# Kernel tuning notes

Hardware: AMD Instinct MI355X
Metric: run time of the kernel (lower is better)

Reference implementation:

```python
import jax, jax.numpy as jnp
import numpy as np

V, E, H, B, T = 32000, 256, 512, 64, 24

def setup_inputs() -> dict:
    key = jax.random.key(0)
    ks = jax.random.split(key, 24)
    def n(k, shape, s=0.02):
        return jax.random.normal(k, shape, dtype=jnp.float32) * s
    inp = {
        "question_feat": n(ks[0], (B, H), 1.0),
        "image_feat": n(ks[1], (B, H), 1.0),
        "answer_seq": jax.random.randint(ks[2], (B, T), 0, V),
        "embedding": n(ks[3], (V, E)),
        "attn_W": n(ks[4], (H, 3 * H)),
        "attn_b": jnp.zeros((H,), jnp.float32),
        "v_W": n(ks[5], (1, H)),
        "fc_W": n(ks[6], (V, H)),
        "fc_b": jnp.zeros((V,), jnp.float32),
    }
    in_sizes = [E + 2 * H, H, H]  # layer0 sees cat(embed, context)=1280
    for l in range(3):
        inp[f"W_ih{l}"] = n(ks[7 + 4 * l], (4 * H, in_sizes[l]))
        inp[f"W_hh{l}"] = n(ks[8 + 4 * l], (4 * H, H))
        inp[f"b_ih{l}"] = jnp.zeros((4 * H,), jnp.float32)
        inp[f"b_hh{l}"] = jnp.zeros((4 * H,), jnp.float32)
    return inp

def _lstm_cell(x, h, c, W_ih, W_hh, b_ih, b_hh):
    # torch gate order: i, f, g, o
    g = x @ W_ih.T + b_ih + h @ W_hh.T + b_hh
    i, f, gg, o = jnp.split(g, 4, axis=-1)
    c_new = jax.nn.sigmoid(f) * c + jax.nn.sigmoid(i) * jnp.tanh(gg)
    h_new = jax.nn.sigmoid(o) * jnp.tanh(c_new)
    return h_new, c_new

def reference(question_feat, image_feat, answer_seq, embedding, attn_W, attn_b, v_W,
              fc_W, fc_b,
              W_ih0, W_hh0, b_ih0, b_hh0,
              W_ih1, W_hh1, b_ih1, b_hh1,
              W_ih2, W_hh2, b_ih2, b_hh2):
    combined = jnp.concatenate([question_feat, image_feat], axis=1)  # [B, 2H]
    x = embedding[answer_seq]            # [B, T, E]
    xs = jnp.swapaxes(x, 0, 1)           # [T, B, E]
    Ws = ((W_ih0, W_hh0, b_ih0, b_hh0),
          (W_ih1, W_hh1, b_ih1, b_hh1),
          (W_ih2, W_hh2, b_ih2, b_hh2))

    def step(carry, x_t):
        h, c, prev_attn = carry          # h, c: [3, B, H]; prev_attn: [B, H]
        energy = jnp.tanh(jnp.concatenate([prev_attn, combined], axis=1) @ attn_W.T + attn_b)
        aw = jax.nn.softmax(energy @ v_W.T, axis=1)  # [B, 1] (softmax over singleton, faithful to source)
        ctx = aw * combined                          # [B, 2H]
        cur = jnp.concatenate([x_t, ctx], axis=1)    # [B, E+2H]
        hs, cs = [], []
        for l in range(3):
            nh, nc = _lstm_cell(cur, h[l], c[l], *Ws[l])
            hs.append(nh); cs.append(nc); cur = nh
        logits = cur @ fc_W.T + fc_b                 # [B, V]
        return (jnp.stack(hs), jnp.stack(cs), cur), logits

    hdim = question_feat.shape[1]
    bsz = question_feat.shape[0]
    h0 = jnp.zeros((3, bsz, hdim), question_feat.dtype)
    c0 = jnp.zeros((3, bsz, hdim), question_feat.dtype)
    _, outs = jax.lax.scan(step, (h0, c0, question_feat), xs)
    return jnp.swapaxes(outs, 0, 1)  # [B, T, V]
```

## Files before the change

### kernel.cpp

```cpp
#include <hip/hip_runtime.h>
#include <hip/hip_bf16.h>
#include <stdint.h>


typedef short bf16x8 __attribute__((ext_vector_type(8)));
typedef float f32x4 __attribute__((ext_vector_type(4)));

#define NLSTM 96
#define NTILE_N 250
#define HSLOT 32768

__device__ __forceinline__ unsigned short f2b(float f) {
    uint32_t u = __builtin_bit_cast(uint32_t, f);
    uint32_t r = u + 0x7FFFu + ((u >> 16) & 1u);
    return (unsigned short)(r >> 16);
}
__device__ __forceinline__ float fsig(float x) {
    float e = __expf(-x);
    return __builtin_amdgcn_rcpf(1.0f + e);
}
__device__ __forceinline__ float ftanh(float x) {
    float e = __expf(-2.0f * x);
    return (1.0f - e) * __builtin_amdgcn_rcpf(1.0f + e);
}

__global__ __launch_bounds__(256) void prep(
    const float* __restrict__ Whh0,
    const float* __restrict__ Wih1, const float* __restrict__ Whh1,
    const float* __restrict__ Wih2, const float* __restrict__ Whh2,
    unsigned short* __restrict__ Wpk,
    const float* __restrict__ qf,
    const float* __restrict__ imf,
    const int* __restrict__ seq,
    const float* __restrict__ emb,
    unsigned short* __restrict__ X,
    unsigned int* __restrict__ flags,
    unsigned short* __restrict__ hst)
{
    int gid = blockIdx.x;
    int tid = threadIdx.x;
    if (gid < 6144) {
        int layer = gid / (32 * 64);
        int rem = gid % (32 * 64);
        int lbid = rem >> 6, r = rem & 63;
        int q = r >> 4, jj = r & 15;
        int grow = q * 512 + lbid * 16 + jj;
        int K = (layer == 0) ? 512 : 1024;
        size_t wbase = (layer == 0) ? 0
                     : (layer == 1) ? (size_t)32 * 64 * 512
                                    : (size_t)32 * 64 * 512 + (size_t)32 * 64 * 1024;
        unsigned short* dst = Wpk + wbase + ((size_t)lbid * 64 + r) * K;
        const float *s0, *s1 = nullptr;
        if (layer == 0)      { s0 = Whh0 + (size_t)grow * 512; }
        else if (layer == 1) { s0 = Wih1 + (size_t)grow * 512; s1 = Whh1 + (size_t)grow * 512; }
        else                 { s0 = Wih2 + (size_t)grow * 512; s1 = Whh2 + (size_t)grow * 512; }
        int half = tid >> 7, k4 = tid & 127;
        const float* src = (half == 0) ? s0 : s1;
        if (src) {
            f32x4 v = *(const f32x4*)&src[k4 * 4];
            unsigned short o[4];
            #pragma unroll
            for (int j = 0; j < 4; ++j) o[j] = f2b(v[j]);
            *(uint64_t*)&dst[half * 512 + k4 * 4] = *(uint64_t*)o;
        }
    } else if (gid < 7680) {
        int r = gid - 6144;
        int t = r >> 6, b = r & 63;
        int tok = seq[b * 24 + t];
        for (int e = tid; e < 1280; e += 256) {
            float v;
            if (e < 256)      v = emb[(size_t)tok * 256 + e];
            else if (e < 768) v = qf[b * 512 + (e - 256)];
            else              v = imf[b * 512 + (e - 768)];
            X[(size_t)r * 1280 + e] = f2b(v);
        }
    } else {
        int z = (gid - 7680) * 256 + tid;
        for (int i = z; i < 9216; i += 2048) flags[i] = 0u;
        unsigned int* h32 = (unsigned int*)hst;
        for (int l = 0; l < 3; ++l) {
            unsigned int* base = h32 + (size_t)l * 25 * (HSLOT / 2);
            for (int i = z; i < HSLOT / 2; i += 2048) base[i] = 0u;
        }
    }
}

__global__ __launch_bounds__(256) void gemm128(
    const unsigned short* __restrict__ A, int lda,
    const float* __restrict__ Wf, int ldb,
    int K,
    const float* __restrict__ bias0,
    const float* __restrict__ bias1,
    float* __restrict__ outf, int ldo, int mblocks, int xcdq)
{
    __shared__ unsigned short lA[128 * 72];
    __shared__ unsigned short lB[128 * 72];
    int lin = blockIdx.x;
    int wg = (lin & 7) * xcdq + (lin >> 3);
    const int m0 = (wg % mblocks) * 128, n0 = (wg / mblocks) * 128;
    const int tid = threadIdx.x;
    const int lane = tid & 63, wid = tid >> 6;
    const int wm = wid >> 1, wn = wid & 1;

    f32x4 acc[4][4] = {};

    for (int kt = 0; kt < K; kt += 64) {
        #pragma unroll
        for (int c = 0; c < 4; ++c) {
            int chunk = tid + c * 256;
            int row = chunk >> 3, kc = (chunk & 7) * 8;
            *(bf16x8*)&lA[row * 72 + kc] =
                *(const bf16x8*)&A[(size_t)(m0 + row) * lda + kt + kc];
            const float* bp = &Wf[(size_t)(n0 + row) * ldb + kt + kc];
            f32x4 v0 = *(const f32x4*)bp;
            f32x4 v1 = *(const f32x4*)(bp + 4);
            unsigned short o[8];
            #pragma unroll
            for (int x = 0; x < 4; ++x) { o[x] = f2b(v0[x]); o[4 + x] = f2b(v1[x]); }
            *(bf16x8*)&lB[row * 72 + kc] = *(bf16x8*)o;
        }
        __syncthreads();
        #pragma unroll
        for (int ks = 0; ks < 64; ks += 32) {
            int kl = ks + ((lane >> 4) << 3);
            bf16x8 af[4], bfr[4];
            #pragma unroll
            for (int i = 0; i < 4; ++i)
                af[i] = *(const bf16x8*)&lA[(wm * 64 + i * 16 + (lane & 15)) * 72 + kl];
            #pragma unroll
            for (int j = 0; j < 4; ++j)
                bfr[j] = *(const bf16x8*)&lB[(wn * 64 + j * 16 + (lane & 15)) * 72 + kl];
            #pragma unroll
            for (int i = 0; i < 4; ++i)
                #pragma unroll
                for (int j = 0; j < 4; ++j)
                    acc[i][j] = __builtin_amdgcn_mfma_f32_16x16x32_bf16(
                        af[i], bfr[j], acc[i][j], 0, 0, 0);
        }
        __syncthreads();
    }

    #pragma unroll
    for (int i = 0; i < 4; ++i) {
        #pragma unroll
        for (int j = 0; j < 4; ++j) {
            int n = n0 + wn * 64 + j * 16 + (lane & 15);
            float bias = bias0[n] + bias1[n];
            #pragma unroll
            for (int r = 0; r < 4; ++r) {
                int m = m0 + wm * 64 + i * 16 + ((lane >> 4) << 2) + r;
                outf[(size_t)m * ldo + n] = acc[i][j][r] + bias;
            }
        }
    }
}

#define ISSUE_CHUNK(buf, kb0)                                                 \
    {                                                                         \
        _Pragma("unroll")                                                     \
        for (int u_ = 0; u_ < 8; ++u_) {                                      \
            int kg_ = (kb0) + u_ * 32 + lk;                                   \
            const unsigned short* hb_ = (kg_ < 512) ? A0 : A1;                \
            int kk_ = kg_ & 511;                                              \
            const unsigned short* ap_ =                                       \
                hb_ + ((kk_ >> 4) << 10) + brow16 + (kk_ & 15);               \
            asm volatile("global_load_dwordx4 %0, %1, off"                    \
                         : "=v"(buf[u_]) : "v"(ap_) : "memory");              \
        }                                                                     \
    }
#define MFMA_CHUNK(buf, kb0)                                                  \
    {                                                                         \
        _Pragma("unroll")                                                     \
        for (int u_ = 0; u_ < 8; ++u_) {                                      \
            int ksl_ = (kb0) + u_ * 32 + lk;                                  \
            _Pragma("unroll")                                                 \
            for (int q_ = 0; q_ < 4; ++q_) {                                  \
                int gx_ = ((ksl_ >> 3) ^ (lrow & 7)) << 3;                    \
                bf16x8 bq_ = *(const bf16x8*)&lb[(q_ * 16 + lrow) * K + gx_]; \
                acc[q_] = __builtin_amdgcn_mfma_f32_16x16x32_bf16(            \
                    buf[u_], bq_, acc[q_], 0, 0, 0);                          \
            }                                                                 \
        }                                                                     \
    }
#define VM_WAIT(n) { asm volatile("s_waitcnt vmcnt(" #n ")" ::: "memory");    \
                     __builtin_amdgcn_sched_barrier(0); }
#define POLL32(fbase)                                                         \
    {                                                                         \
        const unsigned int* fp_ = (fbase);                                    \
        int idx_ = lane & 31;                                                 \
        while (true) {                                                        \
            unsigned v_ = __hip_atomic_load((unsigned int*)&fp_[idx_],        \
                                            __ATOMIC_RELAXED,                 \
                                            __HIP_MEMORY_SCOPE_AGENT);       \
            if (__all(v_ != 0u)) break;                                       \
            __builtin_amdgcn_s_sleep(1);                                      \
        }                                                                     \
    }

__global__ __launch_bounds__(256, 1) void lstm_wave(
    const unsigned short* __restrict__ Wpk,
    const float* __restrict__ G0,
    const float* __restrict__ bih1, const float* __restrict__ bhh1,
    const float* __restrict__ bih2, const float* __restrict__ bhh2,
    unsigned short* __restrict__ hst,
    unsigned int* __restrict__ flags)
{
    extern __shared__ char smem[];
    unsigned short* lb = (unsigned short*)smem;
    const int bid = blockIdx.x;
    const int tid = threadIdx.x;
    const int lane = tid & 63, w = tid >> 6;
    const int lrow = lane & 15, lk = (lane >> 4) * 8;
    const int layer = bid >> 5;
    const int lbid = bid & 31;
    const int j0 = lbid * 16;

    const int K = (layer == 0) ? 512 : 1024;
    const size_t wbase = (layer == 0) ? 0
                       : (layer == 1) ? (size_t)32 * 64 * 512
                                      : (size_t)32 * 64 * 512 + (size_t)32 * 64 * 1024;
    const unsigned short* Wblk = Wpk + wbase + (size_t)lbid * 64 * K;

    {
        const int kshift = (layer == 0) ? 6 : 7;
        const int gm = (K >> 3) - 1;
        const int total = 64 << kshift;
        for (int idx = tid; idx < total; idx += 256) {
            int row = idx >> kshift, g = idx & gm;
            int gx = g ^ (row & 7);
            *(bf16x8*)&lb[row * K + gx * 8] =
                *(const bf16x8*)&Wblk[(size_t)row * K + g * 8];
        }
    }
    __syncthreads();

    unsigned short* hl = hst + (size_t)layer * 25 * HSLOT;
    const unsigned short* hlow =
        (layer > 0) ? hst + (size_t)(layer - 1) * 25 * HSLOT : nullptr;

    float pb[4] = {0.f, 0.f, 0.f, 0.f};
    if (layer == 1) {
        #pragma unroll
        for (int q = 0; q < 4; ++q)
            pb[q] = bih1[q * 512 + j0 + lrow] + bhh1[q * 512 + j0 + lrow];
    } else if (layer == 2) {
        #pragma unroll
        for (int q = 0; q < 4; ++q)
            pb[q] = bih2[q * 512 + j0 + lrow] + bhh2[q * 512 + j0 + lrow];
    }

    float creg[4] = {0.f, 0.f, 0.f, 0.f};
    const int brow16 = (w * 16 + lrow) << 4;

    for (int t = 0; t < 24; ++t) {
        float g0p[16];
        if (layer == 0) {
            const float* gp = G0 + (size_t)t * 64 * 2048;
            #pragma unroll
            for (int r = 0; r < 4; ++r) {
                int b = w * 16 + ((lane >> 4) << 2) + r;
                #pragma unroll
                for (int q = 0; q < 4; ++q)
                    g0p[r * 4 + q] = gp[(size_t)b * 2048 + q * 512 + j0 + lrow];
            }
        }

        const unsigned short* A0 = (layer == 0)
            ? hl + (size_t)t * HSLOT
            : hlow + (size_t)(t + 1) * HSLOT;
        const unsigned short* A1 = (layer == 0)
            ? A0
            : hl + (size_t)t * HSLOT;

        f32x4 acc[4] = {};
        bf16x8 bufA[8], bufB[8], bufC[8], bufD[8];

        if (layer == 0) {
            if (t > 0) POLL32(flags + (t - 1) * 128 + w * 32);
            ISSUE_CHUNK(bufA, 0); ISSUE_CHUNK(bufB, 256);
            VM_WAIT(8); MFMA_CHUNK(bufA, 0);
            VM_WAIT(0); MFMA_CHUNK(bufB, 256);
        } else {
            if (t > 0) POLL32(flags + (layer * 24 + t - 1) * 128 + w * 32);
            ISSUE_CHUNK(bufC, 512); ISSUE_CHUNK(bufD, 768);
            POLL32(flags + ((layer - 1) * 24 + t) * 128 + w * 32);
            ISSUE_CHUNK(bufA, 0); ISSUE_CHUNK(bufB, 256);
            VM_WAIT(24); MFMA_CHUNK(bufC, 512);
            VM_WAIT(16); MFMA_CHUNK(bufD, 768);
            VM_WAIT(8);  MFMA_CHUNK(bufA, 0);
            VM_WAIT(0);  MFMA_CHUNK(bufB, 256);
        }

        unsigned short* hslot = hl + (size_t)(t + 1) * HSLOT + (lbid << 10);
        #pragma unroll
        for (int r = 0; r < 4; ++r) {
            int b = w * 16 + ((lane >> 4) << 2) + r;
            float g[4];
            #pragma unroll
            for (int q = 0; q < 4; ++q) {
                float p = (layer == 0) ? g0p[r * 4 + q] : pb[q];
                g[q] = acc[q][r] + p;
            }
            float ig = fsig(g[0]);
            float fg = fsig(g[1]);
            float gg = ftanh(g[2]);
            float og = fsig(g[3]);
            float cn = fg * creg[r] + ig * gg;
            creg[r] = cn;
            float h = og * ftanh(cn);
            unsigned int hb = (unsigned int)f2b(h);
            unsigned short* hp = hslot + (b << 4) + lrow;
            asm volatile("global_store_short %0, %1, off sc1"
                         :: "v"(hp), "v"(hb) : "memory");
        }
        asm volatile("s_waitcnt vmcnt(0)" ::: "memory");
        if (lane == 0) {
            __hip_atomic_store(&flags[(layer * 24 + t) * 128 + w * 32 + lbid], 1u,
                               __ATOMIC_RELAXED, __HIP_MEMORY_SCOPE_AGENT);
        }
    }
}

#define FC_ISSUE_G(buf, mtv, ks0)                                             \
    {                                                                         \
        _Pragma("unroll")                                                     \
        for (int u_ = 0; u_ < 4; ++u_) {                                      \
            _Pragma("unroll")                                                 \
            for (int i_ = 0; i_ < 4; ++i_) {                                  \
                int rl_ = i_ * 16 + lrow;                                     \
                int k_ = (ks0) + u_ * 32 + lk;                                \
                const unsigned short* ap_ = h2                                \
                    + (size_t)(2 * (mtv) + wm + 1) * HSLOT                    \
                    + ((k_ >> 4) << 10) + (rl_ << 4) + (k_ & 15);             \
                asm volatile("global_load_dwordx4 %0, %1, off"                \
                             : "=v"(buf[u_ * 4 + i_]) : "v"(ap_) : "memory"); \
            }                                                                 \
        }                                                                     \
    }
#define FC_MFMA_G(buf, ks0)                                                   \
    {                                                                         \
        _Pragma("unroll")                                                     \
        for (int u_ = 0; u_ < 4; ++u_) {                                      \
            int ks_ = (ks0) + u_ * 32 + lk;                                   \
            _Pragma("unroll")                                                 \
            for (int jj_ = 0; jj_ < 4; ++jj_) {                               \
                int row_ = wn * 64 + jj_ * 16 + lrow;                         \
                int gx_ = ((ks_ >> 3) ^ (row_ & 7)) << 3;                     \
                bf16x8 bq_ = *(const bf16x8*)&lB[row_ * 512 + gx_];           \
                _Pragma("unroll")                                             \
                for (int i_ = 0; i_ < 4; ++i_)                                \
                    acc[i_][jj_] = __builtin_amdgcn_mfma_f32_16x16x32_bf16(   \
                        buf[u_ * 4 + i_], bq_, acc[i_][jj_], 0, 0, 0);        \
            }                                                                 \
        }                                                                     \
    }
#define FC_STORES                                                             \
    {                                                                         \
        _Pragma("unroll")                                                     \
        for (int i_ = 0; i_ < 4; ++i_) {                                      \
            _Pragma("unroll")                                                 \
            for (int jj_ = 0; jj_ < 4; ++jj_) {                               \
                int n_ = n0 + wn * 64 + jj_ * 16 + lrow;                      \
                float bias_ = fcb[n_];                                        \
                _Pragma("unroll")                                             \
                for (int r_ = 0; r_ < 4; ++r_) {                              \
                    int m_ = m0 + wm * 64 + i_ * 16 + ((lane >> 4) << 2) + r_;\
                    int b_ = m_ & 63, t_ = m_ >> 6;                           \
                    __builtin_nontemporal_store(                              \
                        acc[i_][jj_][r_] + bias_,                             \
                        &out[(size_t)(b_ * 24 + t_) * 32000 + n_]);           \
                }                                                             \
            }                                                                 \
        }                                                                     \
    }

__global__ __launch_bounds__(256, 1) void fc_gemm(
    const unsigned short* __restrict__ hst,
    const float* __restrict__ fcW,
    const float* __restrict__ fcb,
    float* __restrict__ out)
{
    extern __shared__ char smem[];
    unsigned short* lB = (unsigned short*)smem;
    const int tid = threadIdx.x;
    const int lane = tid & 63, w = tid >> 6;
    const int lrow = lane & 15, lk = (lane >> 4) * 8;
    const int wm = w >> 1, wn = w & 1;
    const unsigned short* h2 = hst + (size_t)2 * 25 * HSLOT;
    const int n0 = blockIdx.x * 128;

    for (int idx = tid; idx < 128 * 64; idx += 256) {
        int row = idx >> 6, g = idx & 63;
        const float* bp = &fcW[(size_t)(n0 + row) * 512 + g * 8];
        f32x4 v0 = *(const f32x4*)bp;
        f32x4 v1 = *(const f32x4*)(bp + 4);
        unsigned short o[8];
        #pragma unroll
        for (int x = 0; x < 4; ++x) { o[x] = f2b(v0[x]); o[4 + x] = f2b(v1[x]); }
        *(bf16x8*)&lB[row * 512 + ((g ^ (row & 7)) << 3)] = *(bf16x8*)o;
    }
    __syncthreads();

    bf16x8 gA[16], gB[16];

    {
        const int m0 = 0;
        f32x4 acc[4][4] = {};
        FC_ISSUE_G(gA, 0, 0); FC_ISSUE_G(gB, 0, 128);
        VM_WAIT(16); FC_MFMA_G(gA, 0);
        FC_ISSUE_G(gA, 0, 256);
        VM_WAIT(16); FC_MFMA_G(gB, 128);
        FC_ISSUE_G(gB, 0, 384);
        VM_WAIT(16); FC_MFMA_G(gA, 256);
        VM_WAIT(0);  FC_MFMA_G(gB, 384);
        FC_ISSUE_G(gA, 1, 0); FC_ISSUE_G(gB, 1, 128);
        FC_STORES;
    }

    for (int mt = 1; mt < 12; ++mt) {
        const int m0 = mt * 128;
        f32x4 acc[4][4] = {};
        VM_WAIT(63);
        FC_MFMA_G(gA, 0);
        FC_ISSUE_G(gA, mt, 256);
        FC_MFMA_G(gB, 128);
        FC_ISSUE_G(gB, mt, 384);
        VM_WAIT(16);
        FC_MFMA_G(gA, 256);
        VM_WAIT(0);
        FC_MFMA_G(gB, 384);
        if (mt < 11) { FC_ISSUE_G(gA, mt + 1, 0); FC_ISSUE_G(gB, mt + 1, 128); }
        FC_STORES;
    }
}

extern "C" void kernel_launch(void* const* d_in, const int* in_sizes, int n_in,
                              void* d_out, int out_size, void* d_ws, size_t ws_size,
                              hipStream_t stream) {
    const float* qf  = (const float*)d_in[0];
    const float* imf = (const float*)d_in[1];
    const int*   seq = (const int*)d_in[2];
    const float* emb = (const float*)d_in[3];
    const float* fcW = (const float*)d_in[7];
    const float* fcb = (const float*)d_in[8];
    const float* Wih[3] = {(const float*)d_in[9],  (const float*)d_in[13], (const float*)d_in[17]};
    const float* Whh[3] = {(const float*)d_in[10], (const float*)d_in[14], (const float*)d_in[18]};
    const float* bih[3] = {(const float*)d_in[11], (const float*)d_in[15], (const float*)d_in[19]};
    const float* bhh[3] = {(const float*)d_in[12], (const float*)d_in[16], (const float*)d_in[20]};

    char* ws = (char*)d_ws;
    unsigned short* X     = (unsigned short*)(ws + 0);
    float*          G0    = (float*)(ws + 3932160);
    unsigned short* hst   = (unsigned short*)(ws + 16515072);
    unsigned int*   flags = (unsigned int*)(ws + 21430272);
    unsigned short* Wpk   = (unsigned short*)(ws + 21467136);

    prep<<<7688, 256, 0, stream>>>(
        Whh[0], Wih[1], Whh[1], Wih[2], Whh[2], Wpk,
        qf, imf, seq, emb, X, flags, hst);

    gemm128<<<192, 256, 0, stream>>>(
        X, 1280, Wih[0], 1280, 1280, bih[0], bhh[0], G0, 2048, 12, 192 / 8);

    lstm_wave<<<NLSTM, 256, 131072, stream>>>(
        Wpk, G0, bih[1], bhh[1], bih[2], bhh[2], hst, flags);

    fc_gemm<<<NTILE_N, 256, 131072, stream>>>(
        hst, fcW, fcb, (float*)d_out);
}
```

Measured before the change: 299.6 us.

## Aggregate LSTM step flags per block and relay them to waves via LDS

Cross-block step synchronization moves from one global flag per wave to one global flag per block. Within a block, the last wave to finish a step sets the block flag, counted with an LDS atomic. On the consumer side only wave 0 polls global memory, then releases the other waves through an LDS flag. This cuts global-memory polling traffic and the number of flag stores, but each wave now waits for the whole producer block rather than just its own batch slice, which adds an extra intra-block hop.

```diff
diff --git a/kernel.cpp b/kernel.cpp
--- a/kernel.cpp
+++ b/kernel.cpp
@@ -76,7 +76,7 @@
         }
     } else {
         int z = (gid - 7680) * 256 + tid;
-        for (int i = z; i < 9216; i += 2048) flags[i] = 0u;
+        for (int i = z; i < 2304; i += 2048) flags[i] = 0u;
         unsigned int* h32 = (unsigned int*)hst;
         for (int l = 0; l < 3; ++l) {
             unsigned int* base = h32 + (size_t)l * 25 * (HSLOT / 2);
@@ -196,6 +196,12 @@
             __builtin_amdgcn_s_sleep(1);                                      \
         }                                                                     \
     }
+#define LDS_SPIN(ptr)                                                         \
+    {                                                                         \
+        while (__hip_atomic_load((ptr), __ATOMIC_RELAXED,                     \
+                                 __HIP_MEMORY_SCOPE_WORKGROUP) == 0u)         \
+            __builtin_amdgcn_s_sleep(1);                                      \
+    }
 
 __global__ __launch_bounds__(256, 1) void lstm_wave(
     const unsigned short* __restrict__ Wpk,
@@ -206,6 +212,9 @@
     unsigned int* __restrict__ flags)
 {
     extern __shared__ char smem[];
+    __shared__ unsigned int syncA[24];
+    __shared__ unsigned int syncB[24];
+    __shared__ unsigned int lcnt[24];
     unsigned short* lb = (unsigned short*)smem;
     const int bid = blockIdx.x;
     const int tid = threadIdx.x;
@@ -221,6 +230,7 @@
                                       : (size_t)32 * 64 * 512 + (size_t)32 * 64 * 1024;
     const unsigned short* Wblk = Wpk + wbase + (size_t)lbid * 64 * K;
 
+    if (tid < 24) { syncA[tid] = 0u; syncB[tid] = 0u; lcnt[tid] = 0u; }
     {
         const int kshift = (layer == 0) ? 6 : 7;
         const int gm = (K >> 3) - 1;
@@ -276,14 +286,39 @@
         bf16x8 bufA[8], bufB[8], bufC[8], bufD[8];
 
         if (layer == 0) {
-            if (t > 0) POLL32(flags + (t - 1) * 128 + w * 32);
+            if (t > 0) {
+                if (w == 0) {
+                    POLL32(flags + (t - 1) * 32);
+                    if (lane == 0)
+                        __hip_atomic_store(&syncA[t], 1u, __ATOMIC_RELAXED,
+                                           __HIP_MEMORY_SCOPE_WORKGROUP);
+                } else {
+                    LDS_SPIN(&syncA[t]);
+                }
+            }
             ISSUE_CHUNK(bufA, 0); ISSUE_CHUNK(bufB, 256);
             VM_WAIT(8); MFMA_CHUNK(bufA, 0);
             VM_WAIT(0); MFMA_CHUNK(bufB, 256);
         } else {
-            if (t > 0) POLL32(flags + (layer * 24 + t - 1) * 128 + w * 32);
+            if (t > 0) {
+                if (w == 0) {
+                    POLL32(flags + (layer * 24 + t - 1) * 32);
+                    if (lane == 0)
+                        __hip_atomic_store(&syncA[t], 1u, __ATOMIC_RELAXED,
+                                           __HIP_MEMORY_SCOPE_WORKGROUP);
+                } else {
+                    LDS_SPIN(&syncA[t]);
+                }
+            }
             ISSUE_CHUNK(bufC, 512); ISSUE_CHUNK(bufD, 768);
-            POLL32(flags + ((layer - 1) * 24 + t) * 128 + w * 32);
+            if (w == 0) {
+                POLL32(flags + ((layer - 1) * 24 + t) * 32);
+                if (lane == 0)
+                    __hip_atomic_store(&syncB[t], 1u, __ATOMIC_RELAXED,
+                                       __HIP_MEMORY_SCOPE_WORKGROUP);
+            } else {
+                LDS_SPIN(&syncB[t]);
+            }
             ISSUE_CHUNK(bufA, 0); ISSUE_CHUNK(bufB, 256);
             VM_WAIT(24); MFMA_CHUNK(bufC, 512);
             VM_WAIT(16); MFMA_CHUNK(bufD, 768);
@@ -315,8 +350,11 @@
         }
         asm volatile("s_waitcnt vmcnt(0)" ::: "memory");
         if (lane == 0) {
-            __hip_atomic_store(&flags[(layer * 24 + t) * 128 + w * 32 + lbid], 1u,
-                               __ATOMIC_RELAXED, __HIP_MEMORY_SCOPE_AGENT);
+            unsigned old = __hip_atomic_fetch_add(&lcnt[t], 1u, __ATOMIC_RELAXED,
+                                                  __HIP_MEMORY_SCOPE_WORKGROUP);
+            if (old == 3u)
+                __hip_atomic_store(&flags[(layer * 24 + t) * 32 + lbid], 1u,
+                                   __ATOMIC_RELAXED, __HIP_MEMORY_SCOPE_AGENT);
         }
     }
 }
```

Result: no change. 295.7 us (-1.3%).
